# Kernel tuning notes

Hardware: AMD Instinct MI355X
Metric: run time of the kernel (lower is better)

Reference implementation:

```python
import jax, jax.numpy as jnp
import numpy as np
import math

STAGE_NUM = 5


def _l2norm(t, axis):
    return t / (1e-6 + jnp.linalg.norm(t, axis=axis, keepdims=True))


def setup_inputs() -> dict:
    key = jax.random.key(0)
    ks = jax.random.split(key, 6)
    b, n, c, h, w, k = 8, 5, 512, 32, 32, 64
    x = jax.random.normal(ks[0], (b, n, c, h, w), dtype=jnp.float32)
    mu = jax.random.normal(ks[1], (1, c, k), dtype=jnp.float32) * math.sqrt(2.0 / k)
    mu = _l2norm(mu, axis=1)
    # 1x1 convs init: normal(0, sqrt(2/(1*1*out_channels)))
    std = math.sqrt(2.0 / c)
    conv1_w = jax.random.normal(ks[2], (c, c), dtype=jnp.float32) * std  # [out,in]
    conv1_b = jnp.zeros((c,), dtype=jnp.float32)
    conv2_w = jax.random.normal(ks[3], (c, c), dtype=jnp.float32) * std
    bn_gamma = jnp.ones((c,), dtype=jnp.float32)
    bn_beta = jnp.zeros((c,), dtype=jnp.float32)
    return {"x": x, "mu": mu, "conv1_w": conv1_w, "conv1_b": conv1_b,
            "conv2_w": conv2_w, "bn_gamma": bn_gamma, "bn_beta": bn_beta}


def reference(x, mu, conv1_w, conv1_b, conv2_w, bn_gamma, bn_beta):
    b, n, c, h, w = x.shape
    xf = x.reshape(b * n, c, h, w)
    idn = xf
    # conv1: 1x1 conv with bias
    y = jnp.einsum('bchw,dc->bdhw', xf, conv1_w) + conv1_b[None, :, None, None]
    # [b, c, N] with N = n*h*w
    y = y.reshape(b, n, c, h, w).transpose(0, 2, 1, 3, 4).reshape(b, c, n * h * w)
    mu_b = jnp.broadcast_to(mu, (b, c, mu.shape[2]))
    z = None
    # EM iterations (no_grad in original; fwd-only so just compute)
    for _ in range(STAGE_NUM):
        z = jax.nn.softmax(jnp.einsum('bcn,bck->bnk', y, mu_b), axis=2)  # [b,N,k]
        z_ = z / (1e-6 + z.sum(axis=1, keepdims=True))
        mu_b = _l2norm(jnp.einsum('bcn,bnk->bck', y, z_), axis=1)
    # reconstruction: mu @ z^T -> [b,c,N]
    rec = jnp.einsum('bck,bnk->bcn', mu_b, z)
    rec = jax.nn.relu(rec.reshape(b, c, n, h, w))
    rec = rec.transpose(0, 2, 1, 3, 4).reshape(b * n, c, h, w)
    # conv2 (no bias) + BatchNorm (training-mode batch stats)
    y2 = jnp.einsum('bchw,dc->bdhw', rec, conv2_w)
    mean = y2.mean(axis=(0, 2, 3), keepdims=True)
    var = y2.var(axis=(0, 2, 3), keepdims=True)
    y2 = (y2 - mean) * jax.lax.rsqrt(var + 1e-5)
    y2 = y2 * bn_gamma[None, :, None, None] + bn_beta[None, :, None, None]
    out = jax.nn.relu(y2 + idn).reshape(b, n, c, h, w)
    return out, mu_b
```

## Files before the change

kernel.cpp:

```cpp
#include <hip/hip_runtime.h>
#include <math.h>

#define CH 512
#define K 64
#define BB 8
#define NIMG 5
#define HW 1024
#define NP 5120
#define BI 40

typedef __attribute__((ext_vector_type(8))) _Float16 f16x8;
typedef __attribute__((ext_vector_type(4))) _Float16 f16x4;
typedef __attribute__((ext_vector_type(4))) float f32x4;
typedef __attribute__((ext_vector_type(8))) short s16x8;

#define AS1 __attribute__((address_space(1)))
#define AS3 __attribute__((address_space(3)))

__global__ __launch_bounds__(256) void wconv(const float* __restrict__ w,
                                             _Float16* __restrict__ o)
{
    int i = blockIdx.x * 256 + threadIdx.x;
    o[i] = (_Float16)w[i];
}

__global__ __launch_bounds__(256) void transpose_f16(
    const float* __restrict__ in, _Float16* __restrict__ out, int P)
{
    __shared__ float tile[64][65];
    int t = threadIdx.x;
    int p0 = blockIdx.x * 64, c0 = blockIdx.y * 64;
    long ibase = (long)blockIdx.z * CH * P;
    long obase = (long)blockIdx.z * P * CH;
    int pl = t & 63, chh = t >> 6;
    #pragma unroll
    for (int i = 0; i < 16; ++i)
        tile[chh + i * 4][pl] = in[ibase + (long)(c0 + chh + i * 4) * P + p0 + pl];
    __syncthreads();
    int cc = t & 31, pr = t >> 5;
    #pragma unroll
    for (int i = 0; i < 8; ++i) {
        int p = pr + i * 8;
        _Float16 lo = (_Float16)tile[cc * 2][p];
        _Float16 hi = (_Float16)tile[cc * 2 + 1][p];
        unsigned lob = (unsigned)*(unsigned short*)&lo;
        unsigned hib = (unsigned)*(unsigned short*)&hi;
        *(unsigned*)&out[obase + (long)(p0 + p) * CH + c0 + cc * 2] = lob | (hib << 16);
    }
}

__global__ __launch_bounds__(256) void bcast_mu2(const float* __restrict__ mu_in,
                                                 float* __restrict__ mu_cur,
                                                 _Float16* __restrict__ muT)
{
    int i = blockIdx.x * 256 + threadIdx.x;
    float v = mu_in[i & 32767];
    mu_cur[i] = v;
    int b = i >> 15, ck = i & 32767, c = ck >> 6, k = ck & 63;
    muT[((long)b << 15) + k * CH + c] = (_Float16)v;
}

__global__ __launch_bounds__(256) void conv_tile(
    const _Float16* __restrict__ Wh, const _Float16* __restrict__ inT,
    const float* __restrict__ bias, float* __restrict__ y2,
    _Float16* __restrict__ y16, _Float16* __restrict__ yT16,
    float* __restrict__ stats, float* __restrict__ statsq, int mode)
{
    __shared__ _Float16 Wt[2][128 * 64];
    __shared__ _Float16 Xt[2][128 * 64];
    int t = threadIdx.x;
    int lane = t & 63, w = t >> 6;
    int l15 = lane & 15, l4 = lane >> 4;
    int wd = w & 1, wp = w >> 1;
    int bi = blockIdx.z;
    int d0 = blockIdx.y * 128;
    int pl0 = blockIdx.x * 128;
    long prow0 = (long)bi * HW + pl0;
    int ci_row = lane >> 3;
    int colb_phys = (lane & 7) * 16;

    f32x4 acc[4][4];
    #pragma unroll
    for (int ai = 0; ai < 4; ++ai)
        #pragma unroll
        for (int bj = 0; bj < 4; ++bj) acc[ai][bj] = (f32x4){0.f, 0.f, 0.f, 0.f};

#define STAGE(buf, cc0)                                                          \
    {                                                                            \
        _Pragma("unroll")                                                        \
        for (int i = 0; i < 4; ++i) {                                            \
            int row = w * 32 + i * 8 + ci_row;                                   \
            int cb = colb_phys ^ ((row & 7) << 4);                               \
            const _Float16* srcW = Wh + (long)(d0 + row) * CH + (cc0) + (cb >> 1);\
            const _Float16* srcX = inT + (prow0 + row) * (long)CH + (cc0) + (cb >> 1);\
            __builtin_amdgcn_global_load_lds((const AS1 void*)srcW,              \
                (AS3 void*)&Wt[buf][(w * 32 + i * 8) * 64], 16, 0, 0);           \
            __builtin_amdgcn_global_load_lds((const AS1 void*)srcX,              \
                (AS3 void*)&Xt[buf][(w * 32 + i * 8) * 64], 16, 0, 0);           \
        }                                                                        \
    }

    STAGE(0, 0)
    __syncthreads();
    for (int c0 = 0; c0 < CH; c0 += 64) {
        int cur = (c0 >> 6) & 1;
        if (c0 + 64 < CH) STAGE(cur ^ 1, c0 + 64)
        #pragma unroll
        for (int kk = 0; kk < 2; ++kk) {
            f16x8 af[4], bf[4];
            #pragma unroll
            for (int ai = 0; ai < 4; ++ai) {
                int row = wd * 64 + ai * 16 + l15;
                int cb = (kk * 64 + l4 * 16) ^ ((row & 7) << 4);
                af[ai] = *(const f16x8*)((const char*)&Wt[cur][0] + row * 128 + cb);
            }
            #pragma unroll
            for (int bj = 0; bj < 4; ++bj) {
                int row = wp * 64 + bj * 16 + l15;
                int cb = (kk * 64 + l4 * 16) ^ ((row & 7) << 4);
                bf[bj] = *(const f16x8*)((const char*)&Xt[cur][0] + row * 128 + cb);
            }
            #pragma unroll
            for (int ai = 0; ai < 4; ++ai)
                #pragma unroll
                for (int bj = 0; bj < 4; ++bj)
                    acc[ai][bj] = __builtin_amdgcn_mfma_f32_16x16x32_f16(
                        af[ai], bf[bj], acc[ai][bj], 0, 0, 0);
        }
        __syncthreads();
    }
#undef STAGE

    int b = bi / NIMG, n = bi % NIMG;
    if (mode == 0) {
        #pragma unroll
        for (int ai = 0; ai < 4; ++ai) {
            int dd = d0 + wd * 64 + ai * 16 + l4 * 4;
            float b0 = bias[dd], b1 = bias[dd + 1], b2 = bias[dd + 2], b3 = bias[dd + 3];
            #pragma unroll
            for (int bj = 0; bj < 4; ++bj) {
                int pb = n * HW + pl0 + wp * 64 + bj * 16 + l15;
                f16x4 pk = { (_Float16)(acc[ai][bj][0] + b0), (_Float16)(acc[ai][bj][1] + b1),
                             (_Float16)(acc[ai][bj][2] + b2), (_Float16)(acc[ai][bj][3] + b3) };
                *(f16x4*)&yT16[((long)b * NP + pb) * CH + dd] = pk;
                long yb = ((long)b * CH + dd) * NP + pb;
                y16[yb] = pk[0];
                y16[yb + NP] = pk[1];
                y16[yb + 2 * NP] = pk[2];
                y16[yb + 3 * NP] = pk[3];
            }
        }
    } else {
        long obase = (long)bi * CH * HW;
        #pragma unroll
        for (int ai = 0; ai < 4; ++ai) {
            int dd = d0 + wd * 64 + ai * 16 + l4 * 4;
            #pragma unroll
            for (int bj = 0; bj < 4; ++bj) {
                int p = pl0 + wp * 64 + bj * 16 + l15;
                long o = obase + (long)dd * HW + p;
                y2[o] = acc[ai][bj][0];
                y2[o + HW] = acc[ai][bj][1];
                y2[o + 2 * HW] = acc[ai][bj][2];
                y2[o + 3 * HW] = acc[ai][bj][3];
            }
        }
        #pragma unroll
        for (int ai = 0; ai < 4; ++ai) {
            #pragma unroll
            for (int i = 0; i < 4; ++i) {
                float s = acc[ai][0][i] + acc[ai][1][i] + acc[ai][2][i] + acc[ai][3][i];
                float q = acc[ai][0][i] * acc[ai][0][i] + acc[ai][1][i] * acc[ai][1][i]
                        + acc[ai][2][i] * acc[ai][2][i] + acc[ai][3][i] * acc[ai][3][i];
                #pragma unroll
                for (int off = 1; off < 16; off <<= 1) {
                    s += __shfl_xor(s, off, 64);
                    q += __shfl_xor(q, off, 64);
                }
                if (l15 == 0) {
                    int dd = d0 + wd * 64 + ai * 16 + l4 * 4 + i;
                    atomicAdd(&stats[dd], s);
                    atomicAdd(&statsq[dd], q);
                }
            }
        }
    }
}

__global__ __launch_bounds__(256) void stage_z_mfma(
    const _Float16* __restrict__ yT, const _Float16* __restrict__ muT,
    _Float16* __restrict__ zT, _Float16* __restrict__ z16,
    float* __restrict__ zsum, int writeZ)
{
    __shared__ _Float16 ms[32768];
    int t = threadIdx.x;
    int w = t >> 6, lane = t & 63, l15 = lane & 15, l4 = lane >> 4;
    int p0 = blockIdx.x * 64;
    int b = blockIdx.y;
    const _Float16* mb = muT + ((long)b << 15);
    #pragma unroll
    for (int it = 0; it < 16; ++it) {
        int sl = t + it * 256;
        int cc = sl >> 8, j = (sl >> 6) & 3, ln = sl & 63;
        int rl15 = ln & 15, rl4 = ln >> 4;
        *(s16x8*)&ms[sl * 8] = *(const s16x8*)&mb[(rl15 + 16 * j) * CH + cc * 32 + rl4 * 8];
    }
    const _Float16* arow = yT + ((long)b * NP + p0 + w * 16 + l15) * CH + l4 * 8;
    f32x4 acc[4];
    #pragma unroll
    for (int j = 0; j < 4; ++j) acc[j] = (f32x4){0.f, 0.f, 0.f, 0.f};
    __syncthreads();
    #pragma unroll
    for (int cc = 0; cc < 16; ++cc) {
        f16x8 a = *(const f16x8*)(arow + cc * 32);
        #pragma unroll
        for (int j = 0; j < 4; ++j) {
            f16x8 bj = *(const f16x8*)&ms[((cc * 4 + j) * 64 + lane) * 8];
            acc[j] = __builtin_amdgcn_mfma_f32_16x16x32_f16(a, bj, acc[j], 0, 0, 0);
        }
    }
    float zv[4][4];
    #pragma unroll
    for (int i = 0; i < 4; ++i) {
        float m = fmaxf(fmaxf(acc[0][i], acc[1][i]), fmaxf(acc[2][i], acc[3][i]));
        #pragma unroll
        for (int off = 1; off < 16; off <<= 1) m = fmaxf(m, __shfl_xor(m, off, 64));
        float e0 = __expf(acc[0][i] - m);
        float e1 = __expf(acc[1][i] - m);
        float e2 = __expf(acc[2][i] - m);
        float e3 = __expf(acc[3][i] - m);
        float s = e0 + e1 + e2 + e3;
        #pragma unroll
        for (int off = 1; off < 16; off <<= 1) s += __shfl_xor(s, off, 64);
        float inv = 1.f / s;
        zv[0][i] = e0 * inv; zv[1][i] = e1 * inv; zv[2][i] = e2 * inv; zv[3][i] = e3 * inv;
    }
    int prow = p0 + w * 16 + l4 * 4;
    long ztbase = (long)b * K * NP;
    #pragma unroll
    for (int j = 0; j < 4; ++j) {
        f16x4 pk = { (_Float16)zv[j][0], (_Float16)zv[j][1],
                     (_Float16)zv[j][2], (_Float16)zv[j][3] };
        *(f16x4*)&zT[ztbase + (long)(l15 + 16 * j) * NP + prow] = pk;
    }
    if (writeZ) {
        long zbase = (long)b * NP * K;
        #pragma unroll
        for (int j = 0; j < 4; ++j)
            #pragma unroll
            for (int i = 0; i < 4; ++i)
                z16[zbase + (long)(prow + i) * K + l15 + 16 * j] = (_Float16)zv[j][i];
    }
    float part[4];
    #pragma unroll
    for (int j = 0; j < 4; ++j) {
        part[j] = zv[j][0] + zv[j][1] + zv[j][2] + zv[j][3];
        part[j] += __shfl_xor(part[j], 16, 64);
        part[j] += __shfl_xor(part[j], 32, 64);
    }
    __syncthreads();
    float* zred = (float*)ms;
    if (l4 == 0) {
        #pragma unroll
        for (int j = 0; j < 4; ++j) zred[w * 64 + l15 + 16 * j] = part[j];
    }
    __syncthreads();
    if (t < 64)
        atomicAdd(&zsum[b * 64 + t], zred[t] + zred[64 + t] + zred[128 + t] + zred[192 + t]);
}

__global__ __launch_bounds__(256) void stage_mu_mfma(
    const _Float16* __restrict__ y16, const _Float16* __restrict__ zT,
    float* __restrict__ macc)
{
    __shared__ _Float16 zs[4096];
    int t = threadIdx.x;
    int w = t >> 6, lane = t & 63, l15 = lane & 15, l4 = lane >> 4;
    int pc = blockIdx.x, ct = blockIdx.y, b = blockIdx.z;
    int pbase = pc * 640;
    const _Float16* zsrc = zT + (long)b * K * NP + (long)(l15 + 16 * w) * NP + l4 * 8;
    const _Float16* arow = y16 + ((long)b * CH + ct * 64 + w * 16 + l15) * NP + l4 * 8;
    f32x4 acc[4];
    #pragma unroll
    for (int j = 0; j < 4; ++j) acc[j] = (f32x4){0.f, 0.f, 0.f, 0.f};
    for (int p0 = pbase; p0 < pbase + 640; p0 += 64) {
        __syncthreads();
        *(s16x8*)&zs[t * 8] = *(const s16x8*)(zsrc + p0);
        *(s16x8*)&zs[2048 + t * 8] = *(const s16x8*)(zsrc + p0 + 32);
        __syncthreads();
        f16x8 a0 = *(const f16x8*)(arow + p0);
        f16x8 a1 = *(const f16x8*)(arow + p0 + 32);
        #pragma unroll
        for (int j = 0; j < 4; ++j) {
            f16x8 bj0 = *(const f16x8*)&zs[(j * 64 + lane) * 8];
            acc[j] = __builtin_amdgcn_mfma_f32_16x16x32_f16(a0, bj0, acc[j], 0, 0, 0);
            f16x8 bj1 = *(const f16x8*)&zs[2048 + (j * 64 + lane) * 8];
            acc[j] = __builtin_amdgcn_mfma_f32_16x16x32_f16(a1, bj1, acc[j], 0, 0, 0);
        }
    }
    float* mp = macc + ((long)pc * BB + b) * K * CH;
    #pragma unroll
    for (int j = 0; j < 4; ++j)
        *(f32x4*)&mp[(long)(l15 + 16 * j) * CH + ct * 64 + w * 16 + l4 * 4] = acc[j];
}

__global__ __launch_bounds__(256) void mu_norm2(
    const float* __restrict__ macc, const float* __restrict__ zsum,
    float* __restrict__ mu_cur, _Float16* __restrict__ mu16,
    _Float16* __restrict__ muT)
{
    int gw = blockIdx.x * 4 + (threadIdx.x >> 6);
    int lane = threadIdx.x & 63;
    int b = gw >> 6, k = gw & 63;
    float v[8];
    float s = 0.f;
    #pragma unroll
    for (int ci = 0; ci < 8; ++ci) {
        int c = ci * 64 + lane;
        float a = 0.f;
        #pragma unroll
        for (int pcc = 0; pcc < 8; ++pcc)
            a += macc[(((long)pcc * BB + b) * K + k) * CH + c];
        v[ci] = a; s += a * a;
    }
    #pragma unroll
    for (int off = 1; off < 64; off <<= 1) s += __shfl_xor(s, off, 64);
    float d = 1e-6f + zsum[b * 64 + k];
    float scale = 1.f / (1e-6f * d + sqrtf(s));
    long mb = (long)b << 15;
    #pragma unroll
    for (int ci = 0; ci < 8; ++ci) {
        int c = ci * 64 + lane;
        float m = v[ci] * scale;
        mu_cur[mb + (long)c * K + k] = m;
        mu16[mb + (long)c * K + k] = (_Float16)m;
        muT[mb + (long)k * CH + c] = (_Float16)m;
    }
}

__global__ __launch_bounds__(256) void rec_mfma(
    const _Float16* __restrict__ z16, const _Float16* __restrict__ mu16,
    _Float16* __restrict__ recT)
{
    __shared__ _Float16 rt[64 * 80];
    int t = threadIdx.x;
    int w = t >> 6, lane = t & 63, l15 = lane & 15, l4 = lane >> 4;
    int p0 = blockIdx.x * 64, ct = blockIdx.y, b = blockIdx.z;
    const _Float16* zb = z16 + (long)b * NP * K;
    const _Float16* mb = mu16 + ((long)b << 15) + (long)(ct * 64 + w * 16 + l15) * K + l4 * 8;
    f32x4 acc[4];
    #pragma unroll
    for (int pj = 0; pj < 4; ++pj) acc[pj] = (f32x4){0.f, 0.f, 0.f, 0.f};
    #pragma unroll
    for (int kc = 0; kc < 64; kc += 32) {
        f16x8 bfr = *(const f16x8*)(mb + kc);
        #pragma unroll
        for (int pj = 0; pj < 4; ++pj) {
            f16x8 a = *(const f16x8*)(zb + (long)(p0 + pj * 16 + l15) * K + kc + l4 * 8);
            acc[pj] = __builtin_amdgcn_mfma_f32_16x16x32_f16(a, bfr, acc[pj], 0, 0, 0);
        }
    }
    #pragma unroll
    for (int pj = 0; pj < 4; ++pj)
        #pragma unroll
        for (int i = 0; i < 4; ++i)
            rt[(pj * 16 + l4 * 4 + i) * 80 + w * 16 + l15] = (_Float16)fmaxf(acc[pj][i], 0.f);
    __syncthreads();
    #pragma unroll
    for (int it = 0; it < 2; ++it) {
        int l = t + it * 256;
        int row = l >> 3, s8 = l & 7;
        *(s16x8*)&recT[((long)b * NP + p0 + row) * CH + ct * 64 + s8 * 8] =
            *(const s16x8*)&rt[row * 80 + s8 * 8];
    }
}

__global__ __launch_bounds__(256) void final_kernel(
    const float* __restrict__ y2, const float* __restrict__ x,
    const float* __restrict__ stats, const float* __restrict__ statsq,
    const float* __restrict__ gamma, const float* __restrict__ beta,
    const float* __restrict__ mu_cur, float* __restrict__ out)
{
    long i4 = (long)blockIdx.x * 256 + threadIdx.x;
    const long NMAIN4 = (long)BI * CH * HW / 4;
    if (i4 < NMAIN4) {
        long i = i4 * 4;
        int d = (int)((i >> 10) & (CH - 1));
        float s = stats[d], sq = statsq[d];
        const float inv = 1.f / (float)(BI * HW);
        float mean = s * inv;
        float var = sq * inv - mean * mean;
        float rs = rsqrtf(var + 1e-5f);
        float g = rs * gamma[d];
        float bb = beta[d] - mean * g;
        float4 yv = *(const float4*)&y2[i];
        float4 xv = *(const float4*)&x[i];
        float4 ov;
        ov.x = fmaxf(yv.x * g + bb + xv.x, 0.f);
        ov.y = fmaxf(yv.y * g + bb + xv.y, 0.f);
        ov.z = fmaxf(yv.z * g + bb + xv.z, 0.f);
        ov.w = fmaxf(yv.w * g + bb + xv.w, 0.f);
        *(float4*)&out[i] = ov;
    } else {
        long j = (i4 - NMAIN4) * 4;
        *(float4*)&out[(long)BI * CH * HW + j] = *(const float4*)&mu_cur[j];
    }
}

extern "C" void kernel_launch(void* const* d_in, const int* in_sizes, int n_in,
                              void* d_out, int out_size, void* d_ws, size_t ws_size,
                              hipStream_t stream) {
    const float* x   = (const float*)d_in[0];
    const float* mu0 = (const float*)d_in[1];
    const float* w1  = (const float*)d_in[2];
    const float* b1  = (const float*)d_in[3];
    const float* w2  = (const float*)d_in[4];
    const float* gm  = (const float*)d_in[5];
    const float* bt  = (const float*)d_in[6];
    float* out = (float*)d_out;

    float* ws = (float*)d_ws;
    _Float16* y16h  = (_Float16*)(ws);
    _Float16* yT16h = (_Float16*)(ws + 10485760);
    _Float16* xTh   = (_Float16*)(ws + 20971520);
    _Float16* zTh   = (_Float16*)(ws + 20971520);
    _Float16* z16h  = (_Float16*)(ws + 22282240);
    float*    macc  = ws + 23592960;
    float*    mu_cur = ws + 31457280;
    _Float16* Wh1   = (_Float16*)(ws + 31719424);
    _Float16* Wh2   = (_Float16*)(ws + 31850496);
    _Float16* mu16h = (_Float16*)(ws + 31981568);
    _Float16* muTh  = (_Float16*)(ws + 32112640);
    float*    zsum  = ws + 32243712;
    float*    stats = ws + 32246272;
    float*    statsq = ws + 32246784;
    float* y2 = out;

    hipMemsetAsync(zsum, 0, 3584 * sizeof(float), stream);

    wconv<<<1024, 256, 0, stream>>>(w1, Wh1);
    wconv<<<1024, 256, 0, stream>>>(w2, Wh2);
    transpose_f16<<<dim3(16, 8, 40), 256, 0, stream>>>(x, xTh, HW);
    conv_tile<<<dim3(8, 4, 40), 256, 0, stream>>>(Wh1, xTh, b1, nullptr, y16h, yT16h,
                                                  nullptr, nullptr, 0);
    bcast_mu2<<<1024, 256, 0, stream>>>(mu0, mu_cur, muTh);

    for (int s = 0; s < 5; ++s) {
        stage_z_mfma<<<dim3(80, 8), 256, 0, stream>>>(yT16h, muTh, zTh, z16h,
                                                      zsum + s * 512, s == 4);
        stage_mu_mfma<<<dim3(8, 8, 8), 256, 0, stream>>>(y16h, zTh, macc);
        mu_norm2<<<128, 256, 0, stream>>>(macc, zsum + s * 512, mu_cur, mu16h, muTh);
    }

    rec_mfma<<<dim3(80, 8, 8), 256, 0, stream>>>(z16h, mu16h, yT16h);
    conv_tile<<<dim3(8, 4, 40), 256, 0, stream>>>(Wh2, yT16h, nullptr, y2, nullptr, nullptr,
                                                  stats, statsq, 1);
    long total4 = ((long)BI * CH * HW + (long)BB * CH * K) / 4;
    final_kernel<<<(int)((total4 + 255) / 256), 256, 0, stream>>>(
        y2, x, stats, statsq, gm, bt, mu_cur, out);
}
```

Baseline: 464.7 us.

## Store mu in MFMA fragment layout, drop LDS staging, single-buffer conv

mu is now written by bcast_mu2 and mu_norm2 in a precomputed MFMA-fragment order, so stage_z reads its B operands straight from global memory instead of staging 64KB into LDS. stage_z now handles two 16-row point tiles per wave, which halves its grid. stage_mu drops its LDS staging of z, reads fragments directly from global, and computes 32 channels per wave, which halves its grid in the channel dimension. conv_tile goes from double-buffered LDS to a single buffer with two barriers per k-step, which loses the overlap between global loads and MFMA work.

```diff
diff --git a/kernel.cpp b/kernel.cpp
--- a/kernel.cpp
+++ b/kernel.cpp
@@ -17,6 +17,13 @@
 #define AS1 __attribute__((address_space(1)))
 #define AS3 __attribute__((address_space(3)))
 
+__device__ inline long mufrag_idx(int b, int c, int k) {
+    int cc = c >> 5, l4 = (c >> 3) & 3, e = c & 7;
+    int j = k >> 4, l15 = k & 15;
+    int lane = l4 * 16 + l15;
+    return ((long)b << 15) + (((cc * 4 + j) * 64 + lane) << 3) + e;
+}
+
 __global__ __launch_bounds__(256) void wconv(const float* __restrict__ w,
                                              _Float16* __restrict__ o)
 {
@@ -51,13 +58,13 @@
 
 __global__ __launch_bounds__(256) void bcast_mu2(const float* __restrict__ mu_in,
                                                  float* __restrict__ mu_cur,
-                                                 _Float16* __restrict__ muT)
+                                                 _Float16* __restrict__ muF)
 {
     int i = blockIdx.x * 256 + threadIdx.x;
     float v = mu_in[i & 32767];
     mu_cur[i] = v;
     int b = i >> 15, ck = i & 32767, c = ck >> 6, k = ck & 63;
-    muT[((long)b << 15) + k * CH + c] = (_Float16)v;
+    muF[mufrag_idx(b, c, k)] = (_Float16)v;
 }
 
 __global__ __launch_bounds__(256) void conv_tile(
@@ -66,8 +73,8 @@
     _Float16* __restrict__ y16, _Float16* __restrict__ yT16,
     float* __restrict__ stats, float* __restrict__ statsq, int mode)
 {
-    __shared__ _Float16 Wt[2][128 * 64];
-    __shared__ _Float16 Xt[2][128 * 64];
+    __shared__ _Float16 Wt[128 * 64];
+    __shared__ _Float16 Xt[128 * 64];
     int t = threadIdx.x;
     int lane = t & 63, w = t >> 6;
     int l15 = lane & 15, l4 = lane >> 4;
@@ -85,26 +92,20 @@
         #pragma unroll
         for (int bj = 0; bj < 4; ++bj) acc[ai][bj] = (f32x4){0.f, 0.f, 0.f, 0.f};
 
-#define STAGE(buf, cc0)                                                          \
-    {                                                                            \
-        _Pragma("unroll")                                                        \
-        for (int i = 0; i < 4; ++i) {                                            \
-            int row = w * 32 + i * 8 + ci_row;                                   \
-            int cb = colb_phys ^ ((row & 7) << 4);                               \
-            const _Float16* srcW = Wh + (long)(d0 + row) * CH + (cc0) + (cb >> 1);\
-            const _Float16* srcX = inT + (prow0 + row) * (long)CH + (cc0) + (cb >> 1);\
-            __builtin_amdgcn_global_load_lds((const AS1 void*)srcW,              \
-                (AS3 void*)&Wt[buf][(w * 32 + i * 8) * 64], 16, 0, 0);           \
-            __builtin_amdgcn_global_load_lds((const AS1 void*)srcX,              \
-                (AS3 void*)&Xt[buf][(w * 32 + i * 8) * 64], 16, 0, 0);           \
-        }                                                                        \
-    }
-
-    STAGE(0, 0)
-    __syncthreads();
     for (int c0 = 0; c0 < CH; c0 += 64) {
-        int cur = (c0 >> 6) & 1;
-        if (c0 + 64 < CH) STAGE(cur ^ 1, c0 + 64)
+        __syncthreads();
+        #pragma unroll
+        for (int i = 0; i < 4; ++i) {
+            int row = w * 32 + i * 8 + ci_row;
+            int cb = colb_phys ^ ((row & 7) << 4);
+            const _Float16* srcW = Wh + (long)(d0 + row) * CH + c0 + (cb >> 1);
+            const _Float16* srcX = inT + (prow0 + row) * (long)CH + c0 + (cb >> 1);
+            __builtin_amdgcn_global_load_lds((const AS1 void*)srcW,
+                (AS3 void*)&Wt[(w * 32 + i * 8) * 64], 16, 0, 0);
+            __builtin_amdgcn_global_load_lds((const AS1 void*)srcX,
+                (AS3 void*)&Xt[(w * 32 + i * 8) * 64], 16, 0, 0);
+        }
+        __syncthreads();
         #pragma unroll
         for (int kk = 0; kk < 2; ++kk) {
             f16x8 af[4], bf[4];
@@ -112,13 +113,13 @@
             for (int ai = 0; ai < 4; ++ai) {
                 int row = wd * 64 + ai * 16 + l15;
                 int cb = (kk * 64 + l4 * 16) ^ ((row & 7) << 4);
-                af[ai] = *(const f16x8*)((const char*)&Wt[cur][0] + row * 128 + cb);
+                af[ai] = *(const f16x8*)((const char*)Wt + row * 128 + cb);
             }
             #pragma unroll
             for (int bj = 0; bj < 4; ++bj) {
                 int row = wp * 64 + bj * 16 + l15;
                 int cb = (kk * 64 + l4 * 16) ^ ((row & 7) << 4);
-                bf[bj] = *(const f16x8*)((const char*)&Xt[cur][0] + row * 128 + cb);
+                bf[bj] = *(const f16x8*)((const char*)Xt + row * 128 + cb);
             }
             #pragma unroll
             for (int ai = 0; ai < 4; ++ai)
@@ -127,9 +128,7 @@
                     acc[ai][bj] = __builtin_amdgcn_mfma_f32_16x16x32_f16(
                         af[ai], bf[bj], acc[ai][bj], 0, 0, 0);
         }
-        __syncthreads();
-    }
-#undef STAGE
+    }
 
     int b = bi / NIMG, n = bi % NIMG;
     if (mode == 0) {
@@ -188,78 +187,80 @@
 }
 
 __global__ __launch_bounds__(256) void stage_z_mfma(
-    const _Float16* __restrict__ yT, const _Float16* __restrict__ muT,
+    const _Float16* __restrict__ yT, const _Float16* __restrict__ muF,
     _Float16* __restrict__ zT, _Float16* __restrict__ z16,
     float* __restrict__ zsum, int writeZ)
 {
-    __shared__ _Float16 ms[32768];
+    __shared__ float zred[256];
     int t = threadIdx.x;
     int w = t >> 6, lane = t & 63, l15 = lane & 15, l4 = lane >> 4;
-    int p0 = blockIdx.x * 64;
+    int p0 = blockIdx.x * 128 + w * 32;
     int b = blockIdx.y;
-    const _Float16* mb = muT + ((long)b << 15);
-    #pragma unroll
-    for (int it = 0; it < 16; ++it) {
-        int sl = t + it * 256;
-        int cc = sl >> 8, j = (sl >> 6) & 3, ln = sl & 63;
-        int rl15 = ln & 15, rl4 = ln >> 4;
-        *(s16x8*)&ms[sl * 8] = *(const s16x8*)&mb[(rl15 + 16 * j) * CH + cc * 32 + rl4 * 8];
-    }
-    const _Float16* arow = yT + ((long)b * NP + p0 + w * 16 + l15) * CH + l4 * 8;
-    f32x4 acc[4];
-    #pragma unroll
-    for (int j = 0; j < 4; ++j) acc[j] = (f32x4){0.f, 0.f, 0.f, 0.f};
-    __syncthreads();
+    const _Float16* mf = muF + ((long)b << 15);
+    const _Float16* a0p = yT + ((long)b * NP + p0 + l15) * CH + l4 * 8;
+    const _Float16* a1p = yT + ((long)b * NP + p0 + 16 + l15) * CH + l4 * 8;
+    f32x4 acc[2][4];
+    #pragma unroll
+    for (int pb = 0; pb < 2; ++pb)
+        #pragma unroll
+        for (int j = 0; j < 4; ++j) acc[pb][j] = (f32x4){0.f, 0.f, 0.f, 0.f};
     #pragma unroll
     for (int cc = 0; cc < 16; ++cc) {
-        f16x8 a = *(const f16x8*)(arow + cc * 32);
+        f16x8 a0 = *(const f16x8*)(a0p + cc * 32);
+        f16x8 a1 = *(const f16x8*)(a1p + cc * 32);
         #pragma unroll
         for (int j = 0; j < 4; ++j) {
-            f16x8 bj = *(const f16x8*)&ms[((cc * 4 + j) * 64 + lane) * 8];
-            acc[j] = __builtin_amdgcn_mfma_f32_16x16x32_f16(a, bj, acc[j], 0, 0, 0);
-        }
-    }
-    float zv[4][4];
-    #pragma unroll
-    for (int i = 0; i < 4; ++i) {
-        float m = fmaxf(fmaxf(acc[0][i], acc[1][i]), fmaxf(acc[2][i], acc[3][i]));
-        #pragma unroll
-        for (int off = 1; off < 16; off <<= 1) m = fmaxf(m, __shfl_xor(m, off, 64));
-        float e0 = __expf(acc[0][i] - m);
-        float e1 = __expf(acc[1][i] - m);
-        float e2 = __expf(acc[2][i] - m);
-        float e3 = __expf(acc[3][i] - m);
-        float s = e0 + e1 + e2 + e3;
-        #pragma unroll
-        for (int off = 1; off < 16; off <<= 1) s += __shfl_xor(s, off, 64);
-        float inv = 1.f / s;
-        zv[0][i] = e0 * inv; zv[1][i] = e1 * inv; zv[2][i] = e2 * inv; zv[3][i] = e3 * inv;
-    }
-    int prow = p0 + w * 16 + l4 * 4;
+            f16x8 bj = *(const f16x8*)&mf[(((cc * 4 + j) * 64) + lane) * 8];
+            acc[0][j] = __builtin_amdgcn_mfma_f32_16x16x32_f16(a0, bj, acc[0][j], 0, 0, 0);
+            acc[1][j] = __builtin_amdgcn_mfma_f32_16x16x32_f16(a1, bj, acc[1][j], 0, 0, 0);
+        }
+    }
     long ztbase = (long)b * K * NP;
+    long zbase = (long)b * NP * K;
+    float part[4] = {0.f, 0.f, 0.f, 0.f};
+    #pragma unroll
+    for (int pb = 0; pb < 2; ++pb) {
+        float zv[4][4];
+        #pragma unroll
+        for (int i = 0; i < 4; ++i) {
+            float m = fmaxf(fmaxf(acc[pb][0][i], acc[pb][1][i]),
+                            fmaxf(acc[pb][2][i], acc[pb][3][i]));
+            #pragma unroll
+            for (int off = 1; off < 16; off <<= 1) m = fmaxf(m, __shfl_xor(m, off, 64));
+            float e0 = __expf(acc[pb][0][i] - m);
+            float e1 = __expf(acc[pb][1][i] - m);
+            float e2 = __expf(acc[pb][2][i] - m);
+            float e3 = __expf(acc[pb][3][i] - m);
+            float s = e0 + e1 + e2 + e3;
+            #pragma unroll
+            for (int off = 1; off < 16; off <<= 1) s += __shfl_xor(s, off, 64);
+            float inv = 1.f / s;
+            zv[0][i] = e0 * inv; zv[1][i] = e1 * inv;
+            zv[2][i] = e2 * inv; zv[3][i] = e3 * inv;
+        }
+        int prow = p0 + pb * 16 + l4 * 4;
+        #pragma unroll
+        for (int j = 0; j < 4; ++j) {
+            f16x4 pk = { (_Float16)zv[j][0], (_Float16)zv[j][1],
+                         (_Float16)zv[j][2], (_Float16)zv[j][3] };
+            *(f16x4*)&zT[ztbase + (long)(l15 + 16 * j) * NP + prow] = pk;
+        }
+        if (writeZ) {
+            #pragma unroll
+            for (int j = 0; j < 4; ++j)
+                #pragma unroll
+                for (int i = 0; i < 4; ++i)
+                    z16[zbase + (long)(prow + i) * K + l15 + 16 * j] = (_Float16)zv[j][i];
+        }
+        #pragma unroll
+        for (int j = 0; j < 4; ++j)
+            part[j] += zv[j][0] + zv[j][1] + zv[j][2] + zv[j][3];
+    }
     #pragma unroll
     for (int j = 0; j < 4; ++j) {
-        f16x4 pk = { (_Float16)zv[j][0], (_Float16)zv[j][1],
-                     (_Float16)zv[j][2], (_Float16)zv[j][3] };
-        *(f16x4*)&zT[ztbase + (long)(l15 + 16 * j) * NP + prow] = pk;
-    }
-    if (writeZ) {
-        long zbase = (long)b * NP * K;
-        #pragma unroll
-        for (int j = 0; j < 4; ++j)
-            #pragma unroll
-            for (int i = 0; i < 4; ++i)
-                z16[zbase + (long)(prow + i) * K + l15 + 16 * j] = (_Float16)zv[j][i];
-    }
-    float part[4];
-    #pragma unroll
-    for (int j = 0; j < 4; ++j) {
-        part[j] = zv[j][0] + zv[j][1] + zv[j][2] + zv[j][3];
         part[j] += __shfl_xor(part[j], 16, 64);
         part[j] += __shfl_xor(part[j], 32, 64);
     }
-    __syncthreads();
-    float* zred = (float*)ms;
     if (l4 == 0) {
         #pragma unroll
         for (int j = 0; j < 4; ++j) zred[w * 64 + l15 + 16 * j] = part[j];
@@ -273,41 +274,41 @@
     const _Float16* __restrict__ y16, const _Float16* __restrict__ zT,
     float* __restrict__ macc)
 {
-    __shared__ _Float16 zs[4096];
     int t = threadIdx.x;
     int w = t >> 6, lane = t & 63, l15 = lane & 15, l4 = lane >> 4;
     int pc = blockIdx.x, ct = blockIdx.y, b = blockIdx.z;
+    int c0 = ct * 128 + w * 32;
     int pbase = pc * 640;
-    const _Float16* zsrc = zT + (long)b * K * NP + (long)(l15 + 16 * w) * NP + l4 * 8;
-    const _Float16* arow = y16 + ((long)b * CH + ct * 64 + w * 16 + l15) * NP + l4 * 8;
-    f32x4 acc[4];
-    #pragma unroll
-    for (int j = 0; j < 4; ++j) acc[j] = (f32x4){0.f, 0.f, 0.f, 0.f};
-    for (int p0 = pbase; p0 < pbase + 640; p0 += 64) {
-        __syncthreads();
-        *(s16x8*)&zs[t * 8] = *(const s16x8*)(zsrc + p0);
-        *(s16x8*)&zs[2048 + t * 8] = *(const s16x8*)(zsrc + p0 + 32);
-        __syncthreads();
-        f16x8 a0 = *(const f16x8*)(arow + p0);
-        f16x8 a1 = *(const f16x8*)(arow + p0 + 32);
+    const _Float16* zrow = zT + (long)b * K * NP + (long)l15 * NP + l4 * 8;
+    const _Float16* a0p = y16 + ((long)b * CH + c0 + l15) * NP + l4 * 8;
+    const _Float16* a1p = y16 + ((long)b * CH + c0 + 16 + l15) * NP + l4 * 8;
+    f32x4 acc[2][4];
+    #pragma unroll
+    for (int ci = 0; ci < 2; ++ci)
+        #pragma unroll
+        for (int j = 0; j < 4; ++j) acc[ci][j] = (f32x4){0.f, 0.f, 0.f, 0.f};
+    for (int p0 = pbase; p0 < pbase + 640; p0 += 32) {
+        f16x8 a0 = *(const f16x8*)(a0p + p0);
+        f16x8 a1 = *(const f16x8*)(a1p + p0);
         #pragma unroll
         for (int j = 0; j < 4; ++j) {
-            f16x8 bj0 = *(const f16x8*)&zs[(j * 64 + lane) * 8];
-            acc[j] = __builtin_amdgcn_mfma_f32_16x16x32_f16(a0, bj0, acc[j], 0, 0, 0);
-            f16x8 bj1 = *(const f16x8*)&zs[2048 + (j * 64 + lane) * 8];
-            acc[j] = __builtin_amdgcn_mfma_f32_16x16x32_f16(a1, bj1, acc[j], 0, 0, 0);
+            f16x8 bj = *(const f16x8*)(zrow + (long)(16 * j) * NP + p0);
+            acc[0][j] = __builtin_amdgcn_mfma_f32_16x16x32_f16(a0, bj, acc[0][j], 0, 0, 0);
+            acc[1][j] = __builtin_amdgcn_mfma_f32_16x16x32_f16(a1, bj, acc[1][j], 0, 0, 0);
         }
     }
     float* mp = macc + ((long)pc * BB + b) * K * CH;
     #pragma unroll
-    for (int j = 0; j < 4; ++j)
-        *(f32x4*)&mp[(long)(l15 + 16 * j) * CH + ct * 64 + w * 16 + l4 * 4] = acc[j];
+    for (int ci = 0; ci < 2; ++ci)
+        #pragma unroll
+        for (int j = 0; j < 4; ++j)
+            *(f32x4*)&mp[(long)(l15 + 16 * j) * CH + c0 + ci * 16 + l4 * 4] = acc[ci][j];
 }
 
 __global__ __launch_bounds__(256) void mu_norm2(
     const float* __restrict__ macc, const float* __restrict__ zsum,
     float* __restrict__ mu_cur, _Float16* __restrict__ mu16,
-    _Float16* __restrict__ muT)
+    _Float16* __restrict__ muF)
 {
     int gw = blockIdx.x * 4 + (threadIdx.x >> 6);
     int lane = threadIdx.x & 63;
@@ -334,7 +335,7 @@
         float m = v[ci] * scale;
         mu_cur[mb + (long)c * K + k] = m;
         mu16[mb + (long)c * K + k] = (_Float16)m;
-        muT[mb + (long)k * CH + c] = (_Float16)m;
+        muF[mufrag_idx(b, c, k)] = (_Float16)m;
     }
 }
 
@@ -430,7 +431,7 @@
     _Float16* Wh1   = (_Float16*)(ws + 31719424);
     _Float16* Wh2   = (_Float16*)(ws + 31850496);
     _Float16* mu16h = (_Float16*)(ws + 31981568);
-    _Float16* muTh  = (_Float16*)(ws + 32112640);
+    _Float16* muFh  = (_Float16*)(ws + 32112640);
     float*    zsum  = ws + 32243712;
     float*    stats = ws + 32246272;
     float*    statsq = ws + 32246784;
@@ -443,13 +444,13 @@
     transpose_f16<<<dim3(16, 8, 40), 256, 0, stream>>>(x, xTh, HW);
     conv_tile<<<dim3(8, 4, 40), 256, 0, stream>>>(Wh1, xTh, b1, nullptr, y16h, yT16h,
                                                   nullptr, nullptr, 0);
-    bcast_mu2<<<1024, 256, 0, stream>>>(mu0, mu_cur, muTh);
+    bcast_mu2<<<1024, 256, 0, stream>>>(mu0, mu_cur, muFh);
 
     for (int s = 0; s < 5; ++s) {
-        stage_z_mfma<<<dim3(80, 8), 256, 0, stream>>>(yT16h, muTh, zTh, z16h,
+        stage_z_mfma<<<dim3(40, 8), 256, 0, stream>>>(yT16h, muFh, zTh, z16h,
                                                       zsum + s * 512, s == 4);
-        stage_mu_mfma<<<dim3(8, 8, 8), 256, 0, stream>>>(y16h, zTh, macc);
-        mu_norm2<<<128, 256, 0, stream>>>(macc, zsum + s * 512, mu_cur, mu16h, muTh);
+        stage_mu_mfma<<<dim3(8, 4, 8), 256, 0, stream>>>(y16h, zTh, macc);
+        mu_norm2<<<128, 256, 0, stream>>>(macc, zsum + s * 512, mu_cur, mu16h, muFh);
     }
 
     rec_mfma<<<dim3(80, 8, 8), 256, 0, stream>>>(z16h, mu16h, yT16h);
```

After: 469.9 us. About the same (+1.1%).
